# Kernel tuning notes

Hardware: AMD Instinct MI355X
Metric: run time of the kernel (lower is better)

The kernel has to match this reference:

```python
import jax, jax.numpy as jnp
import numpy as np

NUM_HEADS = 16
NEG = -1e9


def setup_inputs() -> dict:
    key = jax.random.key(0)
    ks = jax.random.split(key, 9)
    B, S, D = 1, 4096, 1024
    s = 1.0 / np.sqrt(D)
    return {
        "x": jax.random.normal(ks[0], (B, S, D), dtype=jnp.float32),
        "wq": jax.random.normal(ks[1], (D, D), dtype=jnp.float32) * s,
        "bq": jax.random.normal(ks[2], (D,), dtype=jnp.float32) * s,
        "wk": jax.random.normal(ks[3], (D, D), dtype=jnp.float32) * s,
        "bk": jax.random.normal(ks[4], (D,), dtype=jnp.float32) * s,
        "wv": jax.random.normal(ks[5], (D, D), dtype=jnp.float32) * s,
        "bv": jax.random.normal(ks[6], (D,), dtype=jnp.float32) * s,
        "wo": jax.random.normal(ks[7], (D, D), dtype=jnp.float32) * s,
        "bo": jax.random.normal(ks[8], (D,), dtype=jnp.float32) * s,
    }


def reference(x, wq, bq, wk, bk, wv, bv, wo, bo):
    B, S, D = x.shape
    H = NUM_HEADS
    hs = D // H
    # torch Linear: y = x @ W^T + b
    q = x @ wq.T + bq
    k = x @ wk.T + bk
    v = x @ wv.T + bv
    # [B, S, D] -> [B, H, S, hs]
    q = q.reshape(B, S, H, hs).transpose(0, 2, 1, 3)
    k = k.reshape(B, S, H, hs).transpose(0, 2, 1, 3)
    v = v.reshape(B, S, H, hs).transpose(0, 2, 1, 3)
    scores = jnp.einsum("bhqd,bhkd->bhqk", q, k) / jnp.sqrt(jnp.asarray(hs, x.dtype))
    causal = jnp.tril(jnp.ones((S, S), dtype=bool))  # True = keep
    scores = jnp.where(causal, scores, jnp.asarray(NEG, x.dtype))
    weights = jax.nn.softmax(scores, axis=-1)
    out = jnp.einsum("bhqk,bhkd->bhqd", weights, v)
    out = out.transpose(0, 2, 1, 3).reshape(B, S, D)
    return out @ wo.T + bo
```

## Files before the change

### kernel.cpp

```cpp
#include <hip/hip_runtime.h>

#define SEQ 4096
#define DM  1024
#define NH  16
#define HS  64
#define LDQK 2048

typedef __attribute__((ext_vector_type(8))) _Float16 f16x8;
typedef __attribute__((ext_vector_type(4))) _Float16 f16x4;
typedef __attribute__((ext_vector_type(4))) float    f32x4;

#define MFMA16(a, b, c) __builtin_amdgcn_mfma_f32_16x16x32_f16((a), (b), (c), 0, 0, 0)

#define AS1(p) ((const __attribute__((address_space(1))) void*)(p))
#define AS3(p) ((__attribute__((address_space(3))) void*)(p))

#define DPP_ROR_F(x, N) __int_as_float(__builtin_amdgcn_update_dpp( \
    0, __float_as_int(x), 0x120 + (N), 0xF, 0xF, false))

__device__ __forceinline__ float red16_add(float x) {
    x += DPP_ROR_F(x, 1);
    x += DPP_ROR_F(x, 2);
    x += DPP_ROR_F(x, 4);
    x += DPP_ROR_F(x, 8);
    return x;
}

__global__ __launch_bounds__(256) void cast_all(
    const float* __restrict__ x,
    const float* __restrict__ wq, const float* __restrict__ wk,
    const float* __restrict__ wv, const float* __restrict__ wo,
    _Float16* __restrict__ xb, _Float16* __restrict__ wqkb,
    _Float16* __restrict__ wvb, _Float16* __restrict__ wob)
{
    const float* s; _Float16* d; int i;
    if (blockIdx.y == 0) {
        s = x; d = xb;
        i = blockIdx.x * 1024 + threadIdx.x * 4;
    } else {
        int wsel = blockIdx.x >> 10;
        int bx   = blockIdx.x & 1023;
        switch (wsel) {
            case 0:  s = wq; d = wqkb;               break;
            case 1:  s = wk; d = wqkb + (1u << 20);  break;
            case 2:  s = wv; d = wvb;                break;
            default: s = wo; d = wob;                break;
        }
        i = bx * 1024 + threadIdx.x * 4;
    }
    float4 v = *reinterpret_cast<const float4*>(s + i);
    f16x4 o = {(_Float16)v.x, (_Float16)v.y, (_Float16)v.z, (_Float16)v.w};
    *reinterpret_cast<f16x4*>(d + i) = o;
}

template <int BM, typename OUT_T>
__device__ __forceinline__ void gemm_core(
    const _Float16* __restrict__ A,
    const _Float16* __restrict__ W,
    const float*    __restrict__ bias,
    int nbase, int bias_row,
    OUT_T* __restrict__ C,
    int N, int K, float scale, int m0, int n0,
    _Float16* As_, _Float16* Bs_)
{
    constexpr int MI = BM / 32;

    const int t    = threadIdx.x;
    const int w    = t >> 6;
    const int lane = t & 63;
    const int q    = lane >> 4;
    const int l    = lane & 15;
    const int wm   = (w & 1) * (BM / 2);
    const int wn   = (w >> 1) * 64;

    const int srow = lane >> 3;
    const int scol = ((lane & 7) ^ (lane >> 3)) * 8;

    f32x4 acc[MI][4];
    #pragma unroll
    for (int i = 0; i < MI; ++i)
        #pragma unroll
        for (int j = 0; j < 4; ++j) acc[i][j] = (f32x4){0.f, 0.f, 0.f, 0.f};

    for (int k0 = 0; k0 < K; k0 += 64) {
        __syncthreads();
        #pragma unroll
        for (int j = 0; j < BM / 32; ++j) {
            int c = w * (BM / 32) + j;
            __builtin_amdgcn_global_load_lds(
                AS1(A + (size_t)(m0 + c * 8 + srow) * K + k0 + scol),
                AS3((char*)As_ + c * 1024), 16, 0, 0);
        }
        #pragma unroll
        for (int j = 0; j < 4; ++j) {
            int c = w * 4 + j;
            __builtin_amdgcn_global_load_lds(
                AS1(W + (size_t)(n0 + c * 8 + srow) * K + k0 + scol),
                AS3((char*)Bs_ + c * 1024), 16, 0, 0);
        }
        __syncthreads();

        #pragma unroll
        for (int ks = 0; ks < 64; ks += 32) {
            f16x8 af[MI], bf[4];
            #pragma unroll
            for (int i = 0; i < MI; ++i) {
                int r = wm + i * 16 + l;
                af[i] = *reinterpret_cast<const f16x8*>(
                    (const char*)As_ + r * 128 +
                    ((((ks >> 3) + q) ^ (l & 7)) << 4));
            }
            #pragma unroll
            for (int j = 0; j < 4; ++j) {
                int r = wn + j * 16 + l;
                bf[j] = *reinterpret_cast<const f16x8*>(
                    (const char*)Bs_ + r * 128 +
                    ((((ks >> 3) + q) ^ (l & 7)) << 4));
            }
            #pragma unroll
            for (int i = 0; i < MI; ++i)
                #pragma unroll
                for (int j = 0; j < 4; ++j)
                    acc[i][j] = MFMA16(af[i], bf[j], acc[i][j]);
        }
    }

    #pragma unroll
    for (int i = 0; i < MI; ++i) {
        #pragma unroll
        for (int j = 0; j < 4; ++j) {
            int gnb = n0 + wn + j * 16 + l;
            float bc2 = bias_row ? 0.f : bias[gnb - nbase];
            #pragma unroll
            for (int r = 0; r < 4; ++r) {
                int gm = m0 + wm + i * 16 + q * 4 + r;
                float bb = bias_row ? bias[gm] : bc2;
                C[(size_t)gm * N + gnb] = (OUT_T)((acc[i][j][r] + bb) * scale);
            }
        }
    }
}

__global__ __launch_bounds__(256, 4) void gemm_qkv(
    const _Float16* __restrict__ xb, const _Float16* __restrict__ wqkb,
    const _Float16* __restrict__ wvb,
    const float* __restrict__ bq, const float* __restrict__ bk,
    const float* __restrict__ bv,
    _Float16* __restrict__ QKb, _Float16* __restrict__ Vtb)
{
    __shared__ _Float16 As[128][64];
    __shared__ _Float16 Bs[128][64];

    const int bid = (blockIdx.x & 7) * 96 + (blockIdx.x >> 3);
    if (bid < 512) {
        const int n0 = (bid & 15) * 128, m0 = (bid >> 4) * 128;
        const float* bias = (n0 < 1024) ? bq : bk;
        const int   nbase = (n0 < 1024) ? 0 : 1024;
        const float scale = (n0 < 1024) ? 0.18033688011112042f : 1.0f;
        gemm_core<128, _Float16>(xb, wqkb, bias, nbase, 0, QKb,
                                 2048, 1024, scale, m0, n0,
                                 &As[0][0], &Bs[0][0]);
    } else {
        const int v = bid - 512;
        const int n0 = (v & 31) * 128, m0 = (v >> 5) * 128;
        gemm_core<128, _Float16>(wvb, xb, bv, 0, 1, Vtb,
                                 4096, 1024, 1.0f, m0, n0,
                                 &As[0][0], &Bs[0][0]);
    }
}

__global__ __launch_bounds__(256, 4) void gemm_o(
    const _Float16* __restrict__ Ab, const _Float16* __restrict__ wob,
    const float* __restrict__ bo, float* __restrict__ out)
{
    __shared__ _Float16 As[64][64];
    __shared__ _Float16 Bs[128][64];
    const int n0 = blockIdx.x * 128, m0 = blockIdx.y * 64;
    gemm_core<64, float>(Ab, wob, bo, 0, 0, out, 1024, 1024, 1.0f, m0, n0,
                         &As[0][0], &Bs[0][0]);
}

#define APAD 72

__global__ __launch_bounds__(256, 4) void attn_mfma(
    const _Float16* __restrict__ Qg,
    const _Float16* __restrict__ Kg,
    const _Float16* __restrict__ Vt,
    _Float16* __restrict__ O)
{
    __shared__ _Float16 Qs[64][APAD];
    __shared__ _Float16 Ks[4][16][APAD];
    __shared__ _Float16 Vs[64][APAD];
    __shared__ _Float16 Ps[64][APAD];

    const int t    = threadIdx.x;
    const int h    = blockIdx.x;
    const int by   = blockIdx.y;
    const int qb   = (by < 32) ? by : 95 - by;
    const int w    = t >> 6;
    const int lane = t & 63;
    const int q    = lane >> 4;
    const int l    = lane & 15;
    const int sr   = t >> 3;
    const int sc   = (t & 7) * 8;
    const int kj   = sr & 3;
    const int kn   = sr >> 2;

    *reinterpret_cast<uint4*>(&Qs[sr][sc]) =
        *reinterpret_cast<const uint4*>(Qg + (size_t)(qb * 64 + sr) * LDQK + h * 64 + sc);
    *reinterpret_cast<uint4*>(&Qs[sr + 32][sc]) =
        *reinterpret_cast<const uint4*>(Qg + (size_t)(qb * 64 + sr + 32) * LDQK + h * 64 + sc);

    uint4 kr0 = *reinterpret_cast<const uint4*>(Kg + (size_t)(sr) * LDQK + h * 64 + sc);
    uint4 kr1 = *reinterpret_cast<const uint4*>(Kg + (size_t)(sr + 32) * LDQK + h * 64 + sc);
    uint4 vr0 = *reinterpret_cast<const uint4*>(Vt + (size_t)(h * 64 + sr) * SEQ + sc);
    uint4 vr1 = *reinterpret_cast<const uint4*>(Vt + (size_t)(h * 64 + sr + 32) * SEQ + sc);

    float l_acc[4] = {0.f, 0.f, 0.f, 0.f};
    f32x4 oacc[4];
    #pragma unroll
    for (int nt = 0; nt < 4; ++nt) oacc[nt] = (f32x4){0.f, 0.f, 0.f, 0.f};

    __syncthreads();
    f16x8 aq0 = *reinterpret_cast<const f16x8*>(&Qs[w * 16 + l][q * 8]);
    f16x8 aq1 = *reinterpret_cast<const f16x8*>(&Qs[w * 16 + l][32 + q * 8]);

    const int qrow_base = qb * 64 + w * 16 + q * 4;

    for (int kt = 0; kt <= qb; ++kt) {
        __syncthreads();
        *reinterpret_cast<uint4*>(&Ks[kj][kn][sc])     = kr0;
        *reinterpret_cast<uint4*>(&Ks[kj][kn + 8][sc]) = kr1;
        *reinterpret_cast<uint4*>(&Vs[sr][sc])         = vr0;
        *reinterpret_cast<uint4*>(&Vs[sr + 32][sc])    = vr1;
        if (kt < qb) {
            kr0 = *reinterpret_cast<const uint4*>(
                Kg + (size_t)((kt + 1) * 64 + sr) * LDQK + h * 64 + sc);
            kr1 = *reinterpret_cast<const uint4*>(
                Kg + (size_t)((kt + 1) * 64 + sr + 32) * LDQK + h * 64 + sc);
            vr0 = *reinterpret_cast<const uint4*>(
                Vt + (size_t)(h * 64 + sr) * SEQ + (kt + 1) * 64 + sc);
            vr1 = *reinterpret_cast<const uint4*>(
                Vt + (size_t)(h * 64 + sr + 32) * SEQ + (kt + 1) * 64 + sc);
        }
        __syncthreads();

        f32x4 s[4];
        __builtin_amdgcn_s_setprio(1);
        #pragma unroll
        for (int jt = 0; jt < 4; ++jt) {
            f16x8 bk0 = *reinterpret_cast<const f16x8*>(&Ks[jt][l][q * 8]);
            f16x8 bk1 = *reinterpret_cast<const f16x8*>(&Ks[jt][l][32 + q * 8]);
            f32x4 z = (f32x4){0.f, 0.f, 0.f, 0.f};
            z = MFMA16(aq0, bk0, z);
            z = MFMA16(aq1, bk1, z);
            s[jt] = z;
        }
        __builtin_amdgcn_s_setprio(0);

        const bool diag = (kt == qb);

        #pragma unroll
        for (int r = 0; r < 4; ++r) {
            float p0 = s[0][r], p1 = s[1][r], p2 = s[2][r], p3 = s[3][r];
            if (diag) {
                const int qg = qrow_base + r;
                const int kg = kt * 64 + 4 * l;
                p0 = (kg + 0 <= qg) ? p0 : -1e30f;
                p1 = (kg + 1 <= qg) ? p1 : -1e30f;
                p2 = (kg + 2 <= qg) ? p2 : -1e30f;
                p3 = (kg + 3 <= qg) ? p3 : -1e30f;
            }
            p0 = __builtin_amdgcn_exp2f(p0 - 4.f);
            p1 = __builtin_amdgcn_exp2f(p1 - 4.f);
            p2 = __builtin_amdgcn_exp2f(p2 - 4.f);
            p3 = __builtin_amdgcn_exp2f(p3 - 4.f);
            l_acc[r] += (p0 + p1) + (p2 + p3);
            f16x4 pk = {(_Float16)p0, (_Float16)p1, (_Float16)p2, (_Float16)p3};
            *reinterpret_cast<f16x4*>(&Ps[w * 16 + q * 4 + r][4 * l]) = pk;
        }

        f16x8 ap0 = *reinterpret_cast<const f16x8*>(&Ps[w * 16 + l][q * 8]);
        f16x8 ap1 = *reinterpret_cast<const f16x8*>(&Ps[w * 16 + l][32 + q * 8]);
        __builtin_amdgcn_s_setprio(1);
        #pragma unroll
        for (int nt = 0; nt < 4; ++nt) {
            f16x8 bv0 = *reinterpret_cast<const f16x8*>(&Vs[nt * 16 + l][q * 8]);
            f16x8 bv1 = *reinterpret_cast<const f16x8*>(&Vs[nt * 16 + l][32 + q * 8]);
            oacc[nt] = MFMA16(ap0, bv0, oacc[nt]);
            oacc[nt] = MFMA16(ap1, bv1, oacc[nt]);
        }
        __builtin_amdgcn_s_setprio(0);
    }

    #pragma unroll
    for (int r = 0; r < 4; ++r) {
        float inv = 1.f / red16_add(l_acc[r]);
        size_t row = (size_t)(qb * 64 + w * 16 + q * 4 + r) * DM + h * 64;
        #pragma unroll
        for (int nt = 0; nt < 4; ++nt)
            O[row + nt * 16 + l] = (_Float16)(oacc[nt][r] * inv);
    }
}

extern "C" void kernel_launch(void* const* d_in, const int* in_sizes, int n_in,
                              void* d_out, int out_size, void* d_ws, size_t ws_size,
                              hipStream_t stream)
{
    const float* x  = (const float*)d_in[0];
    const float* wq = (const float*)d_in[1];
    const float* bq = (const float*)d_in[2];
    const float* wk = (const float*)d_in[3];
    const float* bk = (const float*)d_in[4];
    const float* wv = (const float*)d_in[5];
    const float* bv = (const float*)d_in[6];
    const float* wo = (const float*)d_in[7];
    const float* bo = (const float*)d_in[8];
    float* out = (float*)d_out;

    char* ws = (char*)d_ws;
    _Float16* xb   = (_Float16*)(ws);
    _Float16* wqkb = (_Float16*)(ws + (8ull  << 20));
    _Float16* wvb  = (_Float16*)(ws + (12ull << 20));
    _Float16* wob  = (_Float16*)(ws + (14ull << 20));
    _Float16* QKb  = (_Float16*)(ws + (16ull << 20));
    _Float16* Vtb  = (_Float16*)(ws + (32ull << 20));
    _Float16* Ab   = (_Float16*)(ws + (40ull << 20));

    cast_all<<<dim3(SEQ * DM / 1024, 2), dim3(256), 0, stream>>>(
        x, wq, wk, wv, wo, xb, wqkb, wvb, wob);

    gemm_qkv<<<dim3(768), dim3(256), 0, stream>>>(
        xb, wqkb, wvb, bq, bk, bv, QKb, Vtb);

    attn_mfma<<<dim3(NH, 64), dim3(256), 0, stream>>>(QKb, QKb + 1024, Vtb, Ab);

    gemm_o<<<dim3(DM / 128, SEQ / 64), dim3(256), 0, stream>>>(
        Ab, wob, bo, out);
}
```

Baseline: 205.0 us.

## Fuse fp32-to-fp16 casting into GEMM tile loads and drop cast kernel

Removes the separate cast_all kernel and has the GEMMs read fp32 inputs and weights directly, converting to fp16 while staging tiles into LDS. This saves one launch and a full write plus re-read of fp16 copies of x and the four weight matrices. In exchange, the fp32 paths use register loads and ds_write instead of direct global-to-LDS loads, double the global bytes per tile, and repeat the conversion across every tile that reuses the same data.

```diff
diff --git a/kernel.cpp b/kernel.cpp
--- a/kernel.cpp
+++ b/kernel.cpp
@@ -26,38 +26,11 @@
     return x;
 }
 
-__global__ __launch_bounds__(256) void cast_all(
-    const float* __restrict__ x,
-    const float* __restrict__ wq, const float* __restrict__ wk,
-    const float* __restrict__ wv, const float* __restrict__ wo,
-    _Float16* __restrict__ xb, _Float16* __restrict__ wqkb,
-    _Float16* __restrict__ wvb, _Float16* __restrict__ wob)
-{
-    const float* s; _Float16* d; int i;
-    if (blockIdx.y == 0) {
-        s = x; d = xb;
-        i = blockIdx.x * 1024 + threadIdx.x * 4;
-    } else {
-        int wsel = blockIdx.x >> 10;
-        int bx   = blockIdx.x & 1023;
-        switch (wsel) {
-            case 0:  s = wq; d = wqkb;               break;
-            case 1:  s = wk; d = wqkb + (1u << 20);  break;
-            case 2:  s = wv; d = wvb;                break;
-            default: s = wo; d = wob;                break;
-        }
-        i = bx * 1024 + threadIdx.x * 4;
-    }
-    float4 v = *reinterpret_cast<const float4*>(s + i);
-    f16x4 o = {(_Float16)v.x, (_Float16)v.y, (_Float16)v.z, (_Float16)v.w};
-    *reinterpret_cast<f16x4*>(d + i) = o;
-}
-
-template <int BM, typename OUT_T>
+template <int BM, typename AT, typename BT, typename OUT_T>
 __device__ __forceinline__ void gemm_core(
-    const _Float16* __restrict__ A,
-    const _Float16* __restrict__ W,
-    const float*    __restrict__ bias,
+    const AT* __restrict__ Ap,
+    const BT* __restrict__ Wp,
+    const float* __restrict__ bias,
     int nbase, int bias_row,
     OUT_T* __restrict__ C,
     int N, int K, float scale, int m0, int n0,
@@ -74,7 +47,7 @@
     const int wn   = (w >> 1) * 64;
 
     const int srow = lane >> 3;
-    const int scol = ((lane & 7) ^ (lane >> 3)) * 8;
+    const int scol = ((lane & 7) ^ srow) * 8;
 
     f32x4 acc[MI][4];
     #pragma unroll
@@ -87,16 +60,34 @@
         #pragma unroll
         for (int j = 0; j < BM / 32; ++j) {
             int c = w * (BM / 32) + j;
-            __builtin_amdgcn_global_load_lds(
-                AS1(A + (size_t)(m0 + c * 8 + srow) * K + k0 + scol),
-                AS3((char*)As_ + c * 1024), 16, 0, 0);
+            if constexpr (sizeof(AT) == 2) {
+                __builtin_amdgcn_global_load_lds(
+                    AS1(Ap + (size_t)(c * 8 + srow) * K + k0 + scol),
+                    AS3((char*)As_ + c * 1024), 16, 0, 0);
+            } else {
+                const float* g = (const float*)Ap + (size_t)(c * 8 + srow) * K + k0 + scol;
+                float4 u0 = *reinterpret_cast<const float4*>(g);
+                float4 u1 = *reinterpret_cast<const float4*>(g + 4);
+                f16x8 h = {(_Float16)u0.x, (_Float16)u0.y, (_Float16)u0.z, (_Float16)u0.w,
+                           (_Float16)u1.x, (_Float16)u1.y, (_Float16)u1.z, (_Float16)u1.w};
+                *reinterpret_cast<f16x8*>((char*)As_ + c * 1024 + lane * 16) = h;
+            }
         }
         #pragma unroll
         for (int j = 0; j < 4; ++j) {
             int c = w * 4 + j;
-            __builtin_amdgcn_global_load_lds(
-                AS1(W + (size_t)(n0 + c * 8 + srow) * K + k0 + scol),
-                AS3((char*)Bs_ + c * 1024), 16, 0, 0);
+            if constexpr (sizeof(BT) == 2) {
+                __builtin_amdgcn_global_load_lds(
+                    AS1(Wp + (size_t)(c * 8 + srow) * K + k0 + scol),
+                    AS3((char*)Bs_ + c * 1024), 16, 0, 0);
+            } else {
+                const float* g = (const float*)Wp + (size_t)(c * 8 + srow) * K + k0 + scol;
+                float4 u0 = *reinterpret_cast<const float4*>(g);
+                float4 u1 = *reinterpret_cast<const float4*>(g + 4);
+                f16x8 h = {(_Float16)u0.x, (_Float16)u0.y, (_Float16)u0.z, (_Float16)u0.w,
+                           (_Float16)u1.x, (_Float16)u1.y, (_Float16)u1.z, (_Float16)u1.w};
+                *reinterpret_cast<f16x8*>((char*)Bs_ + c * 1024 + lane * 16) = h;
+            }
         }
         __syncthreads();
 
@@ -142,8 +133,8 @@
 }
 
 __global__ __launch_bounds__(256, 4) void gemm_qkv(
-    const _Float16* __restrict__ xb, const _Float16* __restrict__ wqkb,
-    const _Float16* __restrict__ wvb,
+    const float* __restrict__ x,  const float* __restrict__ wq,
+    const float* __restrict__ wk, const float* __restrict__ wv,
     const float* __restrict__ bq, const float* __restrict__ bk,
     const float* __restrict__ bv,
     _Float16* __restrict__ QKb, _Float16* __restrict__ Vtb)
@@ -154,30 +145,33 @@
     const int bid = (blockIdx.x & 7) * 96 + (blockIdx.x >> 3);
     if (bid < 512) {
         const int n0 = (bid & 15) * 128, m0 = (bid >> 4) * 128;
+        const float* Wp   = (n0 < 1024) ? wq + (size_t)n0 * 1024
+                                        : wk + (size_t)(n0 - 1024) * 1024;
         const float* bias = (n0 < 1024) ? bq : bk;
         const int   nbase = (n0 < 1024) ? 0 : 1024;
         const float scale = (n0 < 1024) ? 0.18033688011112042f : 1.0f;
-        gemm_core<128, _Float16>(xb, wqkb, bias, nbase, 0, QKb,
-                                 2048, 1024, scale, m0, n0,
-                                 &As[0][0], &Bs[0][0]);
+        gemm_core<128, float, float, _Float16>(
+            x + (size_t)m0 * 1024, Wp, bias, nbase, 0, QKb,
+            2048, 1024, scale, m0, n0, &As[0][0], &Bs[0][0]);
     } else {
         const int v = bid - 512;
         const int n0 = (v & 31) * 128, m0 = (v >> 5) * 128;
-        gemm_core<128, _Float16>(wvb, xb, bv, 0, 1, Vtb,
-                                 4096, 1024, 1.0f, m0, n0,
-                                 &As[0][0], &Bs[0][0]);
+        gemm_core<128, float, float, _Float16>(
+            wv + (size_t)m0 * 1024, x + (size_t)n0 * 1024, bv, 0, 1, Vtb,
+            4096, 1024, 1.0f, m0, n0, &As[0][0], &Bs[0][0]);
     }
 }
 
 __global__ __launch_bounds__(256, 4) void gemm_o(
-    const _Float16* __restrict__ Ab, const _Float16* __restrict__ wob,
+    const _Float16* __restrict__ Ab, const float* __restrict__ wo,
     const float* __restrict__ bo, float* __restrict__ out)
 {
     __shared__ _Float16 As[64][64];
     __shared__ _Float16 Bs[128][64];
     const int n0 = blockIdx.x * 128, m0 = blockIdx.y * 64;
-    gemm_core<64, float>(Ab, wob, bo, 0, 0, out, 1024, 1024, 1.0f, m0, n0,
-                         &As[0][0], &Bs[0][0]);
+    gemm_core<64, _Float16, float, float>(
+        Ab + (size_t)m0 * 1024, wo + (size_t)n0 * 1024, bo, 0, 0, out,
+        1024, 1024, 1.0f, m0, n0, &As[0][0], &Bs[0][0]);
 }
 
 #define APAD 72
@@ -319,22 +313,15 @@
     float* out = (float*)d_out;
 
     char* ws = (char*)d_ws;
-    _Float16* xb   = (_Float16*)(ws);
-    _Float16* wqkb = (_Float16*)(ws + (8ull  << 20));
-    _Float16* wvb  = (_Float16*)(ws + (12ull << 20));
-    _Float16* wob  = (_Float16*)(ws + (14ull << 20));
-    _Float16* QKb  = (_Float16*)(ws + (16ull << 20));
-    _Float16* Vtb  = (_Float16*)(ws + (32ull << 20));
-    _Float16* Ab   = (_Float16*)(ws + (40ull << 20));
-
-    cast_all<<<dim3(SEQ * DM / 1024, 2), dim3(256), 0, stream>>>(
-        x, wq, wk, wv, wo, xb, wqkb, wvb, wob);
+    _Float16* QKb = (_Float16*)(ws);
+    _Float16* Vtb = (_Float16*)(ws + (16ull << 20));
+    _Float16* Ab  = (_Float16*)(ws + (24ull << 20));
 
     gemm_qkv<<<dim3(768), dim3(256), 0, stream>>>(
-        xb, wqkb, wvb, bq, bk, bv, QKb, Vtb);
+        x, wq, wk, wv, bq, bk, bv, QKb, Vtb);
 
     attn_mfma<<<dim3(NH, 64), dim3(256), 0, stream>>>(QKb, QKb + 1024, Vtb, Ab);
 
     gemm_o<<<dim3(DM / 128, SEQ / 64), dim3(256), 0, stream>>>(
-        Ab, wob, bo, out);
-}
+        Ab, wo, bo, out);
+}
```

Measured after the change: 227.1 us. 10.8% more time.

## Split attention across waves by key slice, keeping P in registers

Applied to the files above, without the earlier changes.

The attention kernel now gives each wave a 16-key slice of every KV tile, not a 16-query slice. It computes the transposed scores S^T = K·Q^T so the probability fragment can be fed straight into a 16x16x16 MFMA as the A operand, which removes the P round trip through shared memory. Each wave holds partial output accumulators for all 64 queries, and these are reduced across waves through shared memory at the end. The cost is 64 accumulator floats per thread (occupancy hint lowered from 4 to 3), twice as many smaller MFMAs, and a serialized final reduction with extra barriers.

```diff
diff --git a/kernel.cpp b/kernel.cpp
--- a/kernel.cpp
+++ b/kernel.cpp
@@ -10,21 +10,11 @@
 typedef __attribute__((ext_vector_type(4))) _Float16 f16x4;
 typedef __attribute__((ext_vector_type(4))) float    f32x4;
 
-#define MFMA16(a, b, c) __builtin_amdgcn_mfma_f32_16x16x32_f16((a), (b), (c), 0, 0, 0)
+#define MFMA16(a, b, c)  __builtin_amdgcn_mfma_f32_16x16x32_f16((a), (b), (c), 0, 0, 0)
+#define MFMAK16(a, b, c) __builtin_amdgcn_mfma_f32_16x16x16f16((a), (b), (c), 0, 0, 0)
 
 #define AS1(p) ((const __attribute__((address_space(1))) void*)(p))
 #define AS3(p) ((__attribute__((address_space(3))) void*)(p))
-
-#define DPP_ROR_F(x, N) __int_as_float(__builtin_amdgcn_update_dpp( \
-    0, __float_as_int(x), 0x120 + (N), 0xF, 0xF, false))
-
-__device__ __forceinline__ float red16_add(float x) {
-    x += DPP_ROR_F(x, 1);
-    x += DPP_ROR_F(x, 2);
-    x += DPP_ROR_F(x, 4);
-    x += DPP_ROR_F(x, 8);
-    return x;
-}
 
 __global__ __launch_bounds__(256) void cast_all(
     const float* __restrict__ x,
@@ -182,16 +172,19 @@
 
 #define APAD 72
 
-__global__ __launch_bounds__(256, 4) void attn_mfma(
+__global__ __launch_bounds__(256, 3) void attn_mfma(
     const _Float16* __restrict__ Qg,
     const _Float16* __restrict__ Kg,
     const _Float16* __restrict__ Vt,
     _Float16* __restrict__ O)
 {
-    __shared__ _Float16 Qs[64][APAD];
-    __shared__ _Float16 Ks[4][16][APAD];
-    __shared__ _Float16 Vs[64][APAD];
-    __shared__ _Float16 Ps[64][APAD];
+    __shared__ __align__(16) char smem[27648];
+    _Float16 (*Qs)[APAD] = reinterpret_cast<_Float16(*)[APAD]>(smem);
+    _Float16 (*Ks)[APAD] = reinterpret_cast<_Float16(*)[APAD]>(smem + 9216);
+    _Float16 (*Vs)[APAD] = reinterpret_cast<_Float16(*)[APAD]>(smem + 18432);
+    float* Xl = reinterpret_cast<float*>(smem);
+    float* Xd = reinterpret_cast<float*>(smem + 4096);
+    float* Xo = reinterpret_cast<float*>(smem + 9216);
 
     const int t    = threadIdx.x;
     const int h    = blockIdx.x;
@@ -199,12 +192,10 @@
     const int qb   = (by < 32) ? by : 95 - by;
     const int w    = t >> 6;
     const int lane = t & 63;
-    const int q    = lane >> 4;
-    const int l    = lane & 15;
+    const int lo   = lane & 15;
+    const int g    = lane >> 4;
     const int sr   = t >> 3;
     const int sc   = (t & 7) * 8;
-    const int kj   = sr & 3;
-    const int kn   = sr >> 2;
 
     *reinterpret_cast<uint4*>(&Qs[sr][sc]) =
         *reinterpret_cast<const uint4*>(Qg + (size_t)(qb * 64 + sr) * LDQK + h * 64 + sc);
@@ -217,22 +208,27 @@
     uint4 vr1 = *reinterpret_cast<const uint4*>(Vt + (size_t)(h * 64 + sr + 32) * SEQ + sc);
 
     float l_acc[4] = {0.f, 0.f, 0.f, 0.f};
-    f32x4 oacc[4];
-    #pragma unroll
-    for (int nt = 0; nt < 4; ++nt) oacc[nt] = (f32x4){0.f, 0.f, 0.f, 0.f};
+    f32x4 oacc[4][4];
+    #pragma unroll
+    for (int qt = 0; qt < 4; ++qt)
+        #pragma unroll
+        for (int dt = 0; dt < 4; ++dt) oacc[qt][dt] = (f32x4){0.f, 0.f, 0.f, 0.f};
 
     __syncthreads();
-    f16x8 aq0 = *reinterpret_cast<const f16x8*>(&Qs[w * 16 + l][q * 8]);
-    f16x8 aq1 = *reinterpret_cast<const f16x8*>(&Qs[w * 16 + l][32 + q * 8]);
-
-    const int qrow_base = qb * 64 + w * 16 + q * 4;
+
+    f16x8 bq[4][2];
+    #pragma unroll
+    for (int qt = 0; qt < 4; ++qt) {
+        bq[qt][0] = *reinterpret_cast<const f16x8*>(&Qs[qt * 16 + lo][g * 8]);
+        bq[qt][1] = *reinterpret_cast<const f16x8*>(&Qs[qt * 16 + lo][32 + g * 8]);
+    }
 
     for (int kt = 0; kt <= qb; ++kt) {
         __syncthreads();
-        *reinterpret_cast<uint4*>(&Ks[kj][kn][sc])     = kr0;
-        *reinterpret_cast<uint4*>(&Ks[kj][kn + 8][sc]) = kr1;
-        *reinterpret_cast<uint4*>(&Vs[sr][sc])         = vr0;
-        *reinterpret_cast<uint4*>(&Vs[sr + 32][sc])    = vr1;
+        *reinterpret_cast<uint4*>(&Ks[sr][sc])      = kr0;
+        *reinterpret_cast<uint4*>(&Ks[sr + 32][sc]) = kr1;
+        *reinterpret_cast<uint4*>(&Vs[sr][sc])      = vr0;
+        *reinterpret_cast<uint4*>(&Vs[sr + 32][sc]) = vr1;
         if (kt < qb) {
             kr0 = *reinterpret_cast<const uint4*>(
                 Kg + (size_t)((kt + 1) * 64 + sr) * LDQK + h * 64 + sc);
@@ -245,27 +241,26 @@
         }
         __syncthreads();
 
-        f32x4 s[4];
+        f16x8 ak0 = *reinterpret_cast<const f16x8*>(&Ks[w * 16 + lo][g * 8]);
+        f16x8 ak1 = *reinterpret_cast<const f16x8*>(&Ks[w * 16 + lo][32 + g * 8]);
+        f16x4 bv[4];
+        #pragma unroll
+        for (int dt = 0; dt < 4; ++dt)
+            bv[dt] = *reinterpret_cast<const f16x4*>(&Vs[dt * 16 + lo][w * 16 + g * 4]);
+
+        const bool diag = (kt == qb);
+
         __builtin_amdgcn_s_setprio(1);
         #pragma unroll
-        for (int jt = 0; jt < 4; ++jt) {
-            f16x8 bk0 = *reinterpret_cast<const f16x8*>(&Ks[jt][l][q * 8]);
-            f16x8 bk1 = *reinterpret_cast<const f16x8*>(&Ks[jt][l][32 + q * 8]);
+        for (int qt = 0; qt < 4; ++qt) {
             f32x4 z = (f32x4){0.f, 0.f, 0.f, 0.f};
-            z = MFMA16(aq0, bk0, z);
-            z = MFMA16(aq1, bk1, z);
-            s[jt] = z;
-        }
-        __builtin_amdgcn_s_setprio(0);
-
-        const bool diag = (kt == qb);
-
-        #pragma unroll
-        for (int r = 0; r < 4; ++r) {
-            float p0 = s[0][r], p1 = s[1][r], p2 = s[2][r], p3 = s[3][r];
+            z = MFMA16(ak0, bq[qt][0], z);
+            z = MFMA16(ak1, bq[qt][1], z);
+
+            float p0 = z[0], p1 = z[1], p2 = z[2], p3 = z[3];
             if (diag) {
-                const int qg = qrow_base + r;
-                const int kg = kt * 64 + 4 * l;
+                const int qg = qt * 16 + lo;
+                const int kg = w * 16 + g * 4;
                 p0 = (kg + 0 <= qg) ? p0 : -1e30f;
                 p1 = (kg + 1 <= qg) ? p1 : -1e30f;
                 p2 = (kg + 2 <= qg) ? p2 : -1e30f;
@@ -275,31 +270,60 @@
             p1 = __builtin_amdgcn_exp2f(p1 - 4.f);
             p2 = __builtin_amdgcn_exp2f(p2 - 4.f);
             p3 = __builtin_amdgcn_exp2f(p3 - 4.f);
-            l_acc[r] += (p0 + p1) + (p2 + p3);
-            f16x4 pk = {(_Float16)p0, (_Float16)p1, (_Float16)p2, (_Float16)p3};
-            *reinterpret_cast<f16x4*>(&Ps[w * 16 + q * 4 + r][4 * l]) = pk;
-        }
-
-        f16x8 ap0 = *reinterpret_cast<const f16x8*>(&Ps[w * 16 + l][q * 8]);
-        f16x8 ap1 = *reinterpret_cast<const f16x8*>(&Ps[w * 16 + l][32 + q * 8]);
-        __builtin_amdgcn_s_setprio(1);
-        #pragma unroll
-        for (int nt = 0; nt < 4; ++nt) {
-            f16x8 bv0 = *reinterpret_cast<const f16x8*>(&Vs[nt * 16 + l][q * 8]);
-            f16x8 bv1 = *reinterpret_cast<const f16x8*>(&Vs[nt * 16 + l][32 + q * 8]);
-            oacc[nt] = MFMA16(ap0, bv0, oacc[nt]);
-            oacc[nt] = MFMA16(ap1, bv1, oacc[nt]);
+            l_acc[qt] += (p0 + p1) + (p2 + p3);
+
+            f16x4 a = {(_Float16)p0, (_Float16)p1, (_Float16)p2, (_Float16)p3};
+            #pragma unroll
+            for (int dt = 0; dt < 4; ++dt)
+                oacc[qt][dt] = MFMAK16(a, bv[dt], oacc[qt][dt]);
         }
         __builtin_amdgcn_s_setprio(0);
     }
 
-    #pragma unroll
-    for (int r = 0; r < 4; ++r) {
-        float inv = 1.f / red16_add(l_acc[r]);
-        size_t row = (size_t)(qb * 64 + w * 16 + q * 4 + r) * DM + h * 64;
-        #pragma unroll
-        for (int nt = 0; nt < 4; ++nt)
-            O[row + nt * 16 + l] = (_Float16)(oacc[nt][r] * inv);
+    __syncthreads();
+
+    #pragma unroll
+    for (int qt = 0; qt < 4; ++qt)
+        Xl[((w * 4 + qt) * 4 + g) * 16 + lo] = l_acc[qt];
+    __syncthreads();
+    if (t < 64) {
+        float s = 0.f;
+        #pragma unroll
+        for (int v = 0; v < 4; ++v)
+            #pragma unroll
+            for (int gg = 0; gg < 4; ++gg)
+                s += Xl[((v * 4 + (t >> 4)) * 4 + gg) * 16 + (t & 15)];
+        Xd[t] = 1.f / s;
+    }
+    __syncthreads();
+
+    for (int qt = 0; qt < 4; ++qt) {
+        if (w != qt) {
+            int widx = w - (w > qt);
+            #pragma unroll
+            for (int dt = 0; dt < 4; ++dt)
+                *reinterpret_cast<f32x4*>(Xo + ((widx * 4 + dt) * 64 + lane) * 4) =
+                    oacc[qt][dt];
+        }
+        __syncthreads();
+        if (w == qt) {
+            float inv[4];
+            #pragma unroll
+            for (int r = 0; r < 4; ++r) inv[r] = Xd[qt * 16 + g * 4 + r];
+            #pragma unroll
+            for (int dt = 0; dt < 4; ++dt) {
+                f32x4 s = oacc[qt][dt];
+                #pragma unroll
+                for (int widx = 0; widx < 3; ++widx)
+                    s += *reinterpret_cast<const f32x4*>(
+                        Xo + ((widx * 4 + dt) * 64 + lane) * 4);
+                #pragma unroll
+                for (int r = 0; r < 4; ++r)
+                    O[(size_t)(qb * 64 + qt * 16 + g * 4 + r) * DM + h * 64 +
+                      dt * 16 + lo] = (_Float16)(s[r] * inv[r]);
+            }
+        }
+        __syncthreads();
     }
 }
 
```

Result: faster. 199.8 us (median of 2 runs) (-2.6%).
